# Kernel optimization log

Measured on AMD Instinct MI355X. Metric: run time of the kernel, lower is better.

Reference implementation:

```python
import jax, jax.numpy as jnp
import numpy as np

B, L, E = 2, 2048, 1024
H = 16
DH = E // H  # head dim for qk and v (dim_qk=dim_v=embed_dim)
HID = 4 * E  # fcn_dim_factor * dim_v
SCALE = DH ** 0.5


def setup_inputs() -> dict:
    key = jax.random.key(0)
    ks = jax.random.split(key, 12)
    s = lambda fan_in: 1.0 / np.sqrt(fan_in)
    return {
        "x": jax.random.uniform(ks[0], (B, L), jnp.float32),
        "z": jax.random.normal(ks[1], (B, L, E), jnp.float32),
        "Wq": jax.random.normal(ks[2], (E, E), jnp.float32) * s(E),
        "bq": jnp.zeros((E,), jnp.float32),
        "Wk": jax.random.normal(ks[3], (E, E), jnp.float32) * s(E),
        "bk": jnp.zeros((E,), jnp.float32),
        "Wv": jax.random.normal(ks[4], (E, E), jnp.float32) * s(E),
        "bv": jnp.zeros((E,), jnp.float32),
        "W1": jax.random.normal(ks[5], (E, HID), jnp.float32) * s(E),
        "b1": jnp.zeros((HID,), jnp.float32),
        "W2": jax.random.normal(ks[6], (HID, 1), jnp.float32) * s(HID),
        "b2": jnp.zeros((1,), jnp.float32),
    }


def reference(x, z, Wq, bq, Wk, bk, Wv, bv, W1, b1, W2, b2):
    # Projections -> (B, H, L, DH)
    def heads(t):
        return t.reshape(B, L, H, DH).transpose(0, 2, 1, 3)

    Q = heads(z @ Wq + bq)
    K = heads(z @ Wk + bk)
    V = heads(z @ Wv + bv)

    # Scores (B, H, L, L)
    S = jnp.einsum("bhid,bhjd->bhij", Q, K) / SCALE

    # Weighted softmax along query axis (dim=-2), weighted by population x
    w = x[:, None, :, None]  # (B, 1, L, 1), broadcasts over queries i
    m = jnp.max(S, axis=-2, keepdims=True)
    e = w * jnp.exp(S - m)
    A = e / jnp.sum(e, axis=-2, keepdims=True)

    # V scaled by population weight, then AV
    V_scaled = w * V
    O = jnp.einsum("bhij,bhjd->bhid", A, V_scaled)  # (B, H, L, DH)
    O = O.transpose(0, 2, 1, 3).reshape(B, L, H * DH)

    # FFN: Linear -> GELU (exact) -> Linear(->1) -> squeeze
    y = jax.nn.gelu(O @ W1 + b1, approximate=False)
    y = (y @ W2 + b2).squeeze(-1)  # (B, L)
    return y
```

## Files before the change

kernel.cpp:

```cpp
#include <hip/hip_runtime.h>
#include <hip/hip_bf16.h>
#include <math.h>

#define B_    2
#define L_    2048
#define E_    1024
#define H_    16
#define DH_   64
#define HID_  4096
#define NROW_ (B_*L_)
#define BH_   (B_*H_)

#define QSCL  0.18033688011112042f

typedef __attribute__((ext_vector_type(8)))  short    short8v;
typedef _Float16 half8v __attribute__((ext_vector_type(8)));
typedef __attribute__((ext_vector_type(16))) float    f32x16;

#define MFMA32(A, Bv, C) __builtin_amdgcn_mfma_f32_32x32x16_bf16((A), (Bv), (C), 0, 0, 0)
#define MFMAH(A, Bv, C)  __builtin_amdgcn_mfma_f32_32x32x16_f16((A), (Bv), (C), 0, 0, 0)

#define WAITV(N) asm volatile("s_waitcnt vmcnt(" #N ")" ::: "memory")
#define SBAR()   __builtin_amdgcn_s_barrier()

__device__ __forceinline__ unsigned short f2bf(float f) {
    union { float f; unsigned u; } v; v.f = f;
    return (unsigned short)((v.u + 0x8000u) >> 16);
}
__device__ __forceinline__ unsigned pack2_bf16(float lo, float hi) {
    union { float f; unsigned u; } a, b; a.f = lo; b.f = hi;
    return __builtin_amdgcn_perm(b.u + 0x8000u, a.u + 0x8000u, 0x07060302u);
}
__device__ __forceinline__ float bf2f(unsigned short u) {
    union { unsigned u; float f; } v; v.u = ((unsigned)u) << 16;
    return v.f;
}

__device__ __forceinline__ void gl_lds16(const void* g, void* l) {
    __builtin_amdgcn_global_load_lds(
        (const __attribute__((address_space(1))) unsigned int*)g,
        (__attribute__((address_space(3))) unsigned int*)l, 16, 0, 0);
}

__device__ __forceinline__ float erf_fast(float v) {
    float a = fabsf(v);
    float t = __builtin_amdgcn_rcpf(1.0f + 0.3275911f * a);
    float p = t * (0.254829592f + t * (-0.284496736f + t * (1.421413741f +
              t * (-1.453152027f + t * 1.061405429f))));
    float r = 1.0f - p * __expf(-a * a);
    return copysignf(r, v);
}

__global__ __launch_bounds__(256) void zh_prep(
    const float* __restrict__ z, _Float16* __restrict__ zh)
{
    const size_t i = ((size_t)blockIdx.x * 256 + threadIdx.x) * 8;
    float4 a = *(const float4*)&z[i];
    float4 b = *(const float4*)&z[i + 4];
    union { _Float16 h[8]; half8v v; } o;
    o.h[0] = (_Float16)a.x; o.h[1] = (_Float16)a.y;
    o.h[2] = (_Float16)a.z; o.h[3] = (_Float16)a.w;
    o.h[4] = (_Float16)b.x; o.h[5] = (_Float16)b.y;
    o.h[6] = (_Float16)b.z; o.h[7] = (_Float16)b.w;
    *(half8v*)&zh[i] = o.v;
}

__global__ __launch_bounds__(256) void wprep3(
    const float* __restrict__ Wq, const float* __restrict__ Wk,
    const float* __restrict__ Wv,
    _Float16* __restrict__ Tq, _Float16* __restrict__ Tk,
    _Float16* __restrict__ Tv)
{
    const float* src = (blockIdx.z == 0) ? Wq : (blockIdx.z == 1) ? Wk : Wv;
    _Float16*    dst = (blockIdx.z == 0) ? Tq : (blockIdx.z == 1) ? Tk : Tv;
    __shared__ float tile[64][65];
    const int t  = threadIdx.x;
    const int r0 = blockIdx.y * 64, c0 = blockIdx.x * 64;
    #pragma unroll
    for (int u = 0; u < 4; ++u) {
        int f = t + 256 * u, row = f >> 4, c4 = (f & 15) << 2;
        *(float4*)&tile[row][c4] = *(const float4*)&src[(size_t)(r0 + row) * E_ + c0 + c4];
    }
    __syncthreads();
    #pragma unroll
    for (int u = 0; u < 4; ++u) {
        int f = t + 256 * u, c = f >> 4, r4 = (f & 15) << 2;
        union { _Float16 h[4]; uint2 u2; } pk;
        pk.h[0] = (_Float16)tile[r4 + 0][c];
        pk.h[1] = (_Float16)tile[r4 + 1][c];
        pk.h[2] = (_Float16)tile[r4 + 2][c];
        pk.h[3] = (_Float16)tile[r4 + 3][c];
        *(uint2*)&dst[(size_t)(c0 + c) * E_ + r0 + r4] = pk.u2;
    }
}

__global__ __launch_bounds__(256) void w1prep(
    const float* __restrict__ W1, _Float16* __restrict__ W1t)
{
    __shared__ float tile[64][65];
    const int t  = threadIdx.x;
    const int r0 = blockIdx.y * 64, c0 = blockIdx.x * 64;
    #pragma unroll
    for (int u = 0; u < 4; ++u) {
        int f = t + 256 * u, row = f >> 4, c4 = (f & 15) << 2;
        *(float4*)&tile[row][c4] = *(const float4*)&W1[(size_t)(r0 + row) * HID_ + c0 + c4];
    }
    __syncthreads();
    #pragma unroll
    for (int u = 0; u < 4; ++u) {
        int f = t + 256 * u, c = f >> 4, r4 = (f & 15) << 2;
        union { _Float16 h[4]; uint2 u2; } pk;
        pk.h[0] = (_Float16)tile[r4 + 0][c];
        pk.h[1] = (_Float16)tile[r4 + 1][c];
        pk.h[2] = (_Float16)tile[r4 + 2][c];
        pk.h[3] = (_Float16)tile[r4 + 3][c];
        *(uint2*)&W1t[(size_t)(c0 + c) * E_ + r0 + r4] = pk.u2;
    }
}

__global__ __launch_bounds__(256) void qkv_mfma(
    const _Float16* __restrict__ zh,
    const _Float16* __restrict__ Tall,
    const float* __restrict__ bq, const float* __restrict__ bk,
    const float* __restrict__ bv,
    unsigned short* __restrict__ outQKV)
{
    const int which = blockIdx.y >> 3;
    const float* bias = (which == 0) ? bq : (which == 1) ? bk : bv;
    const float  osc  = (which == 0) ? QSCL : 1.0f;
    unsigned short* out = outQKV + (size_t)which * ((size_t)BH_ * L_ * DH_);

    __shared__ _Float16 Ah[2][128 * 64];
    __shared__ _Float16 Bs[2][128 * 64];

    const int t    = threadIdx.x;
    const int lane = t & 63;
    const int w    = t >> 6;
    const int l31  = lane & 31;
    const int hq   = lane >> 5;
    const int wm   = w >> 1, wn = w & 1;
    const int m0   = blockIdx.x * 128;
    const int n0   = blockIdx.y * 128;

    const int srow0 = (lane >> 3);
    const int ssl   = lane & 7;

    f32x16 acc[2][2] = {};

#define QKV_STAGE(bb, kc)                                                          \
    {                                                                              \
        _Pragma("unroll")                                                          \
        for (int u = 0; u < 4; ++u) {                                              \
            int ch  = w * 4 + u;                                                   \
            int row = ch * 8 + srow0;                                              \
            gl_lds16(&zh[(size_t)(m0 + row) * E_ + (kc) * 64 + ((ssl ^ (row & 7)) << 3)], \
                     &Ah[bb][ch * 512]);                                           \
            gl_lds16(&Tall[(size_t)(n0 + row) * E_ + (kc) * 64 + ((ssl ^ (row & 7)) << 3)], \
                     &Bs[bb][ch * 512]);                                           \
        }                                                                          \
    }

    QKV_STAGE(0, 0);
    QKV_STAGE(1, 1);
    __syncthreads();
    int cur = 0;

    for (int kc = 0; kc < 16; ++kc) {
        if (kc < 15) WAITV(8); else WAITV(0);
        SBAR();
        __builtin_amdgcn_s_setprio(1);
        #pragma unroll
        for (int ks = 0; ks < 4; ++ks) {
            half8v fb[2];
            #pragma unroll
            for (int nb = 0; nb < 2; ++nb) {
                int br = wn * 64 + nb * 32 + l31;
                fb[nb] = *(const half8v*)&Bs[cur][br * 64 + (((ks * 2 + hq) ^ (br & 7)) << 3)];
            }
            #pragma unroll
            for (int mb = 0; mb < 2; ++mb) {
                int ar = wm * 64 + mb * 32 + l31;
                half8v fa = *(const half8v*)&Ah[cur][ar * 64 + (((ks * 2 + hq) ^ (ar & 7)) << 3)];
                acc[mb][0] = MFMAH(fa, fb[0], acc[mb][0]);
                acc[mb][1] = MFMAH(fa, fb[1], acc[mb][1]);
            }
        }
        __builtin_amdgcn_s_setprio(0);
        SBAR();
        if (kc + 2 < 16) QKV_STAGE(cur, kc + 2);
        cur ^= 1;
    }

    #pragma unroll
    for (int nb = 0; nb < 2; ++nb) {
        int n  = n0 + wn * 64 + nb * 32 + l31;
        int nn = n & 1023;
        int h  = nn >> 6, dh = nn & 63;
        float bb = bias[nn];
        #pragma unroll
        for (int mb = 0; mb < 2; ++mb) {
            #pragma unroll
            for (int r = 0; r < 16; ++r) {
                int m  = m0 + wm * 64 + mb * 32 + (r & 3) + 8 * (r >> 2) + 4 * hq;
                int b  = m >> 11, i = m & (L_ - 1);
                out[((size_t)(b * H_ + h) * L_ + i) * DH_ + dh] = f2bf((acc[mb][nb][r] + bb) * osc);
            }
        }
    }
#undef QKV_STAGE
}

__global__ __launch_bounds__(256) void col_stats_mfma(
    const unsigned short* __restrict__ Qb, const unsigned short* __restrict__ Kb,
    const float* __restrict__ x, float* __restrict__ Do)
{
    __shared__ unsigned short Qlds[2][128 * 64];
    __shared__ float xlds[L_];

    const int t    = threadIdx.x;
    const int lane = t & 63;
    const int wv   = t >> 6;
    const int l31  = lane & 31;
    const int hq   = lane >> 5;
    const int bh   = blockIdx.y;
    const int b    = bh >> 4;
    const int j0   = blockIdx.x * 256 + wv * 64;

    const int srow0 = (lane >> 3);
    const int ssl   = lane & 7;

    #pragma unroll
    for (int u = 0; u < 2; ++u) {
        int f = t + 256 * u;
        *(float4*)&xlds[f * 4] = *(const float4*)&x[(size_t)b * L_ + f * 4];
    }

    short8v kf[2][4];
    #pragma unroll
    for (int s = 0; s < 2; ++s) {
        const unsigned short* kp = Kb + ((size_t)bh * L_ + j0 + s * 32 + l31) * DH_ + hq * 8;
        #pragma unroll
        for (int c = 0; c < 4; ++c) kf[s][c] = *(const short8v*)(kp + c * 16);
    }

    float d0[16], d1[16];
    #pragma unroll
    for (int r = 0; r < 16; ++r) { d0[r] = 0.f; d1[r] = 0.f; }

#define CS_STAGE(bb, ich)                                                           \
    {                                                                               \
        _Pragma("unroll")                                                           \
        for (int u = 0; u < 4; ++u) {                                               \
            int ch  = wv * 4 + u;                                                   \
            int row = ch * 8 + srow0;                                               \
            gl_lds16(&Qb[((size_t)bh * L_ + (ich) * 128 + row) * DH_ + ((ssl ^ (row & 7)) << 3)], \
                     &Qlds[bb][ch * 512]);                                          \
        }                                                                           \
    }

    CS_STAGE(0, 0);
    CS_STAGE(1, 1);
    __syncthreads();
    int cur = 0;

    const int NT = L_ / 128;
    for (int ich = 0; ich < NT; ++ich) {
        if (ich < NT - 1) WAITV(4); else WAITV(0);
        SBAR();
        #pragma unroll
        for (int cc = 0; cc < 4; ++cc) {
            f32x16 a0 = {}, a1 = {};
            __builtin_amdgcn_s_setprio(1);
            #pragma unroll
            for (int c = 0; c < 4; ++c) {
                int qr = cc * 32 + l31;
                short8v qv = *(const short8v*)&Qlds[cur][qr * 64 + (((c * 2 + hq) ^ (qr & 7)) << 3)];
                a0 = MFMA32(kf[0][c], qv, a0);
                a1 = MFMA32(kf[1][c], qv, a1);
            }
            __builtin_amdgcn_s_setprio(0);
            float xi = xlds[ich * 128 + cc * 32 + l31];
            #pragma unroll
            for (int r = 0; r < 16; ++r) {
                d0[r] += xi * __builtin_amdgcn_exp2f(a0[r]);
                d1[r] += xi * __builtin_amdgcn_exp2f(a1[r]);
            }
        }
        SBAR();
        if (ich + 2 < NT) CS_STAGE(cur, ich + 2);
        cur ^= 1;
    }

    #pragma unroll
    for (int r = 0; r < 16; ++r) {
        #pragma unroll
        for (int off = 16; off > 0; off >>= 1) {
            d0[r] += __shfl_xor(d0[r], off);
            d1[r] += __shfl_xor(d1[r], off);
        }
    }
    if (l31 == 0) {
        #pragma unroll
        for (int r = 0; r < 16; ++r) {
            int jr = 4 * hq + (r & 3) + 8 * (r >> 2);
            Do[(size_t)bh * L_ + j0 + jr]      = d0[r];
            Do[(size_t)bh * L_ + j0 + 32 + jr] = d1[r];
        }
    }
#undef CS_STAGE
}

__global__ __launch_bounds__(256) void vt_prep(
    const unsigned short* __restrict__ Vb, const float* __restrict__ x,
    const float* __restrict__ Do, unsigned short* __restrict__ Vt)
{
    const int bh = blockIdx.y;
    const int b  = bh >> 4;
    const int j  = blockIdx.x * 256 + threadIdx.x;
    const float s = x[(size_t)b * L_ + j] / Do[(size_t)bh * L_ + j];
    const unsigned short* vp = Vb + ((size_t)bh * L_ + j) * DH_;
    #pragma unroll
    for (int c = 0; c < 16; ++c) {
        ushort4 v = *(const ushort4*)&vp[c * 4];
        Vt[((size_t)bh * DH_ + c * 4 + 0) * L_ + j] = f2bf(bf2f(v.x) * s);
        Vt[((size_t)bh * DH_ + c * 4 + 1) * L_ + j] = f2bf(bf2f(v.y) * s);
        Vt[((size_t)bh * DH_ + c * 4 + 2) * L_ + j] = f2bf(bf2f(v.z) * s);
        Vt[((size_t)bh * DH_ + c * 4 + 3) * L_ + j] = f2bf(bf2f(v.w) * s);
    }
}

__global__ __launch_bounds__(512) void attn_out_mfma(
    const unsigned short* __restrict__ Qb, const unsigned short* __restrict__ Kb,
    const unsigned short* __restrict__ Vt, const float* __restrict__ x,
    _Float16* __restrict__ Of)
{
    __shared__ unsigned short Klds[2][2][64 * 64];
    __shared__ unsigned short Vlds[2][2][64 * 64];
    __shared__ float comb[4][64 * 67];

    const int t    = threadIdx.x;
    const int lane = t & 63;
    const int wv   = t >> 6;
    const int iwv  = wv & 3;
    const int jh   = wv >> 2;
    const int l31  = lane & 31;
    const int hq   = lane >> 5;
    const int bh   = blockIdx.y;
    const int b    = bh >> 4, hh = bh & 15;
    const int iw   = blockIdx.x * 256 + iwv * 64;

    const int srow0 = (lane >> 3);
    const int ssl   = lane & 7;

    short8v qf[2][4];
    #pragma unroll
    for (int ig = 0; ig < 2; ++ig) {
        const unsigned short* qp = Qb + ((size_t)bh * L_ + iw + ig * 32 + l31) * DH_ + hq * 8;
        #pragma unroll
        for (int c = 0; c < 4; ++c) qf[ig][c] = *(const short8v*)(qp + c * 16);
    }

    f32x16 accO[2][2] = {};

#define AO_STAGE(bb, jt)                                                            \
    {                                                                               \
        _Pragma("unroll")                                                           \
        for (int u = 0; u < 2; ++u) {                                               \
            int ch  = iwv * 2 + u;                                                  \
            int row = ch * 8 + srow0;                                               \
            gl_lds16(&Kb[((size_t)bh * L_ + (jt) * 64 + row) * DH_ + ((ssl ^ (row & 7)) << 3)], \
                     &Klds[jh][bb][ch * 512]);                                      \
            gl_lds16(&Vt[((size_t)bh * DH_ + row) * L_ + (jt) * 64 + ((ssl ^ (row & 7)) << 3)], \
                     &Vlds[jh][bb][ch * 512]);                                      \
        }                                                                           \
    }

    AO_STAGE(0, jh * 16 + 0);
    AO_STAGE(1, jh * 16 + 1);
    __syncthreads();
    int cur = 0;

    for (int ltj = 0; ltj < 16; ++ltj) {
        if (ltj < 15) WAITV(4); else WAITV(0);
        SBAR();

        uint4 pa[2][4];
        #pragma unroll
        for (int js = 0; js < 2; ++js) {
            f32x16 as0 = {}, as1 = {};
            __builtin_amdgcn_s_setprio(1);
            #pragma unroll
            for (int c = 0; c < 4; ++c) {
                int krow = js * 32 + l31;
                short8v kfr = *(const short8v*)&Klds[jh][cur][krow * 64 + (((c * 2 + hq) ^ (krow & 7)) << 3)];
                as0 = MFMA32(kfr, qf[0][c], as0);
                as1 = MFMA32(kfr, qf[1][c], as1);
            }
            __builtin_amdgcn_s_setprio(0);
            #pragma unroll
            for (int ig = 0; ig < 2; ++ig) {
                const f32x16& as = (ig == 0) ? as0 : as1;
                float p[16];
                #pragma unroll
                for (int r = 0; r < 16; ++r) p[r] = __builtin_amdgcn_exp2f(as[r]);

                unsigned P0 = pack2_bf16(p[0], p[1]);
                unsigned P1 = pack2_bf16(p[2], p[3]);
                unsigned Q0 = pack2_bf16(p[4], p[5]);
                unsigned Q1 = pack2_bf16(p[6], p[7]);
                asm("v_permlane32_swap_b32 %0, %1" : "+v"(P0), "+v"(Q0));
                asm("v_permlane32_swap_b32 %0, %1" : "+v"(P1), "+v"(Q1));
                pa[ig][js * 2 + 0] = make_uint4(P0, P1, Q0, Q1);

                unsigned R0 = pack2_bf16(p[8],  p[9]);
                unsigned R1 = pack2_bf16(p[10], p[11]);
                unsigned S0 = pack2_bf16(p[12], p[13]);
                unsigned S1 = pack2_bf16(p[14], p[15]);
                asm("v_permlane32_swap_b32 %0, %1" : "+v"(R0), "+v"(S0));
                asm("v_permlane32_swap_b32 %0, %1" : "+v"(R1), "+v"(S1));
                pa[ig][js * 2 + 1] = make_uint4(R0, R1, S0, S1);
            }
        }

        __builtin_amdgcn_s_setprio(1);
        #pragma unroll
        for (int c = 0; c < 4; ++c) {
            union { uint4 u; short8v s; } pa0, pa1;
            pa0.u = pa[0][c]; pa1.u = pa[1][c];
            int r0 = l31, r1 = 32 + l31;
            short8v vf0 = *(const short8v*)&Vlds[jh][cur][r0 * 64 + (((c * 2 + hq) ^ (r0 & 7)) << 3)];
            short8v vf1 = *(const short8v*)&Vlds[jh][cur][r1 * 64 + (((c * 2 + hq) ^ (r1 & 7)) << 3)];
            accO[0][0] = MFMA32(pa0.s, vf0, accO[0][0]);
            accO[0][1] = MFMA32(pa0.s, vf1, accO[0][1]);
            accO[1][0] = MFMA32(pa1.s, vf0, accO[1][0]);
            accO[1][1] = MFMA32(pa1.s, vf1, accO[1][1]);
        }
        __builtin_amdgcn_s_setprio(0);
        SBAR();
        if (ltj + 2 < 16) AO_STAGE(cur, jh * 16 + ltj + 2);
        cur ^= 1;
    }

    if (jh == 1) {
        float* cb = &comb[iwv][lane * 67];
        #pragma unroll
        for (int g = 0; g < 2; ++g)
            #pragma unroll
            for (int h = 0; h < 2; ++h)
                #pragma unroll
                for (int r = 0; r < 16; ++r)
                    cb[(g * 2 + h) * 16 + r] = accO[g][h][r];
    }
    __syncthreads();
    if (jh == 0) {
        const float* cb = &comb[iwv][lane * 67];
        #pragma unroll
        for (int g = 0; g < 2; ++g)
            #pragma unroll
            for (int h = 0; h < 2; ++h)
                #pragma unroll
                for (int r = 0; r < 16; ++r)
                    accO[g][h][r] += cb[(g * 2 + h) * 16 + r];

        #pragma unroll
        for (int ig = 0; ig < 2; ++ig) {
            #pragma unroll
            for (int q = 0; q < 4; ++q) {
                float4 xq = *(const float4*)&x[(size_t)b * L_ + iw + ig * 32 + 4 * hq + 8 * q];
                const float xs[4] = { xq.x, xq.y, xq.z, xq.w };
                #pragma unroll
                for (int k = 0; k < 4; ++k) {
                    int r    = q * 4 + k;
                    int irow = iw + ig * 32 + 4 * hq + 8 * q + k;
                    size_t base = ((size_t)b * L_ + irow) * E_ + hh * DH_;
                    Of[base + l31]      = (_Float16)(accO[ig][0][r] * xs[k]);
                    Of[base + 32 + l31] = (_Float16)(accO[ig][1][r] * xs[k]);
                }
            }
        }
    }
#undef AO_STAGE
}

__global__ __launch_bounds__(256) void y_init(float* __restrict__ y, const float* __restrict__ b2)
{
    y[blockIdx.x * 256 + threadIdx.x] = b2[0];
}

__global__ __launch_bounds__(256) void mlp_mfma(
    const _Float16* __restrict__ Of, const _Float16* __restrict__ W1t,
    const float* __restrict__ b1, const float* __restrict__ W2,
    float* __restrict__ y)
{
    __shared__ _Float16 Oh[2][128 * 64];
    __shared__ _Float16 Wh[2][128 * 64];

    const int t    = threadIdx.x;
    const int lane = t & 63;
    const int w    = t >> 6;
    const int l31  = lane & 31;
    const int hq   = lane >> 5;
    const int wm   = w >> 1, wn = w & 1;
    const int m0   = blockIdx.x * 128;
    const int n0   = blockIdx.y * 128;

    const int srow0 = (lane >> 3);
    const int ssl   = lane & 7;

    f32x16 acc[2][2] = {};

#define MLP_STAGE(bb, kc)                                                          \
    {                                                                              \
        _Pragma("unroll")                                                          \
        for (int u = 0; u < 4; ++u) {                                              \
            int ch  = w * 4 + u;                                                   \
            int row = ch * 8 + srow0;                                              \
            gl_lds16(&Of[(size_t)(m0 + row) * E_ + (kc) * 64 + ((ssl ^ (row & 7)) << 3)], \
                     &Oh[bb][ch * 512]);                                           \
            gl_lds16(&W1t[(size_t)(n0 + row) * E_ + (kc) * 64 + ((ssl ^ (row & 7)) << 3)], \
                     &Wh[bb][ch * 512]);                                           \
        }                                                                          \
    }

    MLP_STAGE(0, 0);
    MLP_STAGE(1, 1);
    __syncthreads();
    int cur = 0;

    for (int kc = 0; kc < 16; ++kc) {
        if (kc < 15) WAITV(8); else WAITV(0);
        SBAR();
        __builtin_amdgcn_s_setprio(1);
        #pragma unroll
        for (int ks = 0; ks < 4; ++ks) {
            half8v fb[2];
            #pragma unroll
            for (int nb = 0; nb < 2; ++nb) {
                int br = wn * 64 + nb * 32 + l31;
                fb[nb] = *(const half8v*)&Wh[cur][br * 64 + (((ks * 2 + hq) ^ (br & 7)) << 3)];
            }
            #pragma unroll
            for (int mb = 0; mb < 2; ++mb) {
                int ar = wm * 64 + mb * 32 + l31;
                half8v fa = *(const half8v*)&Oh[cur][ar * 64 + (((ks * 2 + hq) ^ (ar & 7)) << 3)];
                acc[mb][0] = MFMAH(fa, fb[0], acc[mb][0]);
                acc[mb][1] = MFMAH(fa, fb[1], acc[mb][1]);
            }
        }
        __builtin_amdgcn_s_setprio(0);
        SBAR();
        if (kc + 2 < 16) MLP_STAGE(cur, kc + 2);
        cur ^= 1;
    }

    const int hid0 = n0 + wn * 64 + l31;
    const float bb0 = b1[hid0],      w20 = W2[hid0];
    const float bb1 = b1[hid0 + 32], w21 = W2[hid0 + 32];
    #pragma unroll
    for (int mb = 0; mb < 2; ++mb) {
        #pragma unroll
        for (int r = 0; r < 16; ++r) {
            float h0 = acc[mb][0][r] + bb0;
            float h1 = acc[mb][1][r] + bb1;
            float s  = 0.5f * h0 * (1.0f + erf_fast(h0 * 0.70710678f)) * w20
                     + 0.5f * h1 * (1.0f + erf_fast(h1 * 0.70710678f)) * w21;
            #pragma unroll
            for (int off = 16; off > 0; off >>= 1) s += __shfl_xor(s, off);
            if (l31 == 0) {
                int m = m0 + wm * 64 + mb * 32 + (r & 3) + 8 * (r >> 2) + 4 * hq;
                atomicAdd(&y[m], s);
            }
        }
    }
#undef MLP_STAGE
}

extern "C" void kernel_launch(void* const* d_in, const int* in_sizes, int n_in,
                              void* d_out, int out_size, void* d_ws, size_t ws_size,
                              hipStream_t stream)
{
    const float* x  = (const float*)d_in[0];
    const float* z  = (const float*)d_in[1];
    const float* Wq = (const float*)d_in[2];
    const float* bq = (const float*)d_in[3];
    const float* Wk = (const float*)d_in[4];
    const float* bk = (const float*)d_in[5];
    const float* Wv = (const float*)d_in[6];
    const float* bv = (const float*)d_in[7];
    const float* W1 = (const float*)d_in[8];
    const float* b1 = (const float*)d_in[9];
    const float* W2 = (const float*)d_in[10];
    const float* b2 = (const float*)d_in[11];
    float* y = (float*)d_out;

    const size_t NQ = (size_t)BH_ * L_ * DH_;
    unsigned short* p = (unsigned short*)d_ws;
    unsigned short* Qb  = p;  p += NQ;
    unsigned short* Kb  = p;  p += NQ;
    unsigned short* Vb  = p;  p += NQ;
    unsigned short* Vt  = p;  p += NQ;
    _Float16* zh  = (_Float16*)p;  p += (size_t)NROW_ * E_;
    _Float16* Tq  = (_Float16*)p;  p += (size_t)E_ * E_;
    _Float16* Tk  = (_Float16*)p;  p += (size_t)E_ * E_;
    _Float16* Tv  = (_Float16*)p;  p += (size_t)E_ * E_;
    _Float16* W1t = (_Float16*)p;  p += (size_t)HID_ * E_;
    _Float16* Ofp = (_Float16*)p;  p += (size_t)NROW_ * E_;
    float* Dw = (float*)p;

    zh_prep<<<dim3((NROW_ * E_) / (256 * 8)), 256, 0, stream>>>(z, zh);
    wprep3 <<<dim3(E_ / 64, E_ / 64, 3), 256, 0, stream>>>(Wq, Wk, Wv, Tq, Tk, Tv);
    w1prep <<<dim3(HID_ / 64, E_ / 64), 256, 0, stream>>>(W1, W1t);

    qkv_mfma<<<dim3(NROW_ / 128, 3 * E_ / 128), 256, 0, stream>>>(
        zh, Tq, bq, bk, bv, Qb);

    col_stats_mfma<<<dim3(L_ / 256, BH_), 256, 0, stream>>>(Qb, Kb, x, Dw);

    vt_prep<<<dim3(L_ / 256, BH_), 256, 0, stream>>>(Vb, x, Dw, Vt);

    attn_out_mfma<<<dim3(L_ / 256, BH_), 512, 0, stream>>>(Qb, Kb, Vt, x, Ofp);

    y_init<<<dim3(NROW_ / 256), 256, 0, stream>>>(y, b2);

    mlp_mfma<<<dim3(NROW_ / 128, HID_ / 128), 256, 0, stream>>>(
        Ofp, W1t, b1, W2, y);
}
```

Baseline: 207.1 us.

## Split col_stats query range across two wave groups, tile vt_prep transpose, fold y init

col_stats_mfma now runs 512 threads per block, and the query axis is split into two halves handled by separate wave groups. The partial column sums are combined through shared memory, which doubles the waves per block to hide exp and MFMA latency. vt_prep becomes an LDS-tiled transpose with 16-byte vectorized loads and stores, replacing scattered 2-byte strided writes. The y_init kernel is dropped: y is zeroed with a memset and b2 is added by the first column block of mlp_mfma.

```diff
diff --git a/kernel.cpp b/kernel.cpp
--- a/kernel.cpp
+++ b/kernel.cpp
@@ -210,29 +210,30 @@
 #undef QKV_STAGE
 }
 
-__global__ __launch_bounds__(256) void col_stats_mfma(
+__global__ __launch_bounds__(512) void col_stats_mfma(
     const unsigned short* __restrict__ Qb, const unsigned short* __restrict__ Kb,
     const float* __restrict__ x, float* __restrict__ Do)
 {
-    __shared__ unsigned short Qlds[2][128 * 64];
+    __shared__ unsigned short Qlds[2][2][128 * 64];
     __shared__ float xlds[L_];
+    __shared__ float cD[4][64];
 
     const int t    = threadIdx.x;
     const int lane = t & 63;
     const int wv   = t >> 6;
+    const int jwv  = wv & 3;
+    const int ih   = wv >> 2;
     const int l31  = lane & 31;
     const int hq   = lane >> 5;
     const int bh   = blockIdx.y;
     const int b    = bh >> 4;
-    const int j0   = blockIdx.x * 256 + wv * 64;
+    const int j0   = blockIdx.x * 256 + jwv * 64;
 
     const int srow0 = (lane >> 3);
     const int ssl   = lane & 7;
 
-    #pragma unroll
-    for (int u = 0; u < 2; ++u) {
-        int f = t + 256 * u;
-        *(float4*)&xlds[f * 4] = *(const float4*)&x[(size_t)b * L_ + f * 4];
+    {
+        *(float4*)&xlds[t * 4] = *(const float4*)&x[(size_t)b * L_ + t * 4];
     }
 
     short8v kf[2][4];
@@ -247,14 +248,14 @@
     #pragma unroll
     for (int r = 0; r < 16; ++r) { d0[r] = 0.f; d1[r] = 0.f; }
 
-#define CS_STAGE(bb, ich)                                                           \
+#define CS_STAGE(bb, lt)                                                            \
     {                                                                               \
         _Pragma("unroll")                                                           \
         for (int u = 0; u < 4; ++u) {                                               \
-            int ch  = wv * 4 + u;                                                   \
+            int ch  = jwv * 4 + u;                                                  \
             int row = ch * 8 + srow0;                                               \
-            gl_lds16(&Qb[((size_t)bh * L_ + (ich) * 128 + row) * DH_ + ((ssl ^ (row & 7)) << 3)], \
-                     &Qlds[bb][ch * 512]);                                          \
+            gl_lds16(&Qb[((size_t)bh * L_ + (size_t)(ih * 8 + (lt)) * 128 + row) * DH_ + ((ssl ^ (row & 7)) << 3)], \
+                     &Qlds[ih][bb][ch * 512]);                                      \
         }                                                                           \
     }
 
@@ -263,9 +264,8 @@
     __syncthreads();
     int cur = 0;
 
-    const int NT = L_ / 128;
-    for (int ich = 0; ich < NT; ++ich) {
-        if (ich < NT - 1) WAITV(4); else WAITV(0);
+    for (int lt = 0; lt < 8; ++lt) {
+        if (lt < 7) WAITV(4); else WAITV(0);
         SBAR();
         #pragma unroll
         for (int cc = 0; cc < 4; ++cc) {
@@ -274,12 +274,12 @@
             #pragma unroll
             for (int c = 0; c < 4; ++c) {
                 int qr = cc * 32 + l31;
-                short8v qv = *(const short8v*)&Qlds[cur][qr * 64 + (((c * 2 + hq) ^ (qr & 7)) << 3)];
+                short8v qv = *(const short8v*)&Qlds[ih][cur][qr * 64 + (((c * 2 + hq) ^ (qr & 7)) << 3)];
                 a0 = MFMA32(kf[0][c], qv, a0);
                 a1 = MFMA32(kf[1][c], qv, a1);
             }
             __builtin_amdgcn_s_setprio(0);
-            float xi = xlds[ich * 128 + cc * 32 + l31];
+            float xi = xlds[(ih * 8 + lt) * 128 + cc * 32 + l31];
             #pragma unroll
             for (int r = 0; r < 16; ++r) {
                 d0[r] += xi * __builtin_amdgcn_exp2f(a0[r]);
@@ -287,7 +287,7 @@
             }
         }
         SBAR();
-        if (ich + 2 < NT) CS_STAGE(cur, ich + 2);
+        if (lt + 2 < 8) CS_STAGE(cur, lt + 2);
         cur ^= 1;
     }
 
@@ -299,12 +299,21 @@
             d1[r] += __shfl_xor(d1[r], off);
         }
     }
-    if (l31 == 0) {
+    if (ih == 1 && l31 == 0) {
         #pragma unroll
         for (int r = 0; r < 16; ++r) {
             int jr = 4 * hq + (r & 3) + 8 * (r >> 2);
-            Do[(size_t)bh * L_ + j0 + jr]      = d0[r];
-            Do[(size_t)bh * L_ + j0 + 32 + jr] = d1[r];
+            cD[jwv][jr]      = d0[r];
+            cD[jwv][32 + jr] = d1[r];
+        }
+    }
+    __syncthreads();
+    if (ih == 0 && l31 == 0) {
+        #pragma unroll
+        for (int r = 0; r < 16; ++r) {
+            int jr = 4 * hq + (r & 3) + 8 * (r >> 2);
+            Do[(size_t)bh * L_ + j0 + jr]      = d0[r] + cD[jwv][jr];
+            Do[(size_t)bh * L_ + j0 + 32 + jr] = d1[r] + cD[jwv][32 + jr];
         }
     }
 #undef CS_STAGE
@@ -314,18 +323,41 @@
     const unsigned short* __restrict__ Vb, const float* __restrict__ x,
     const float* __restrict__ Do, unsigned short* __restrict__ Vt)
 {
+    __shared__ float sc[64];
+    __shared__ unsigned short vt[64][66];
+
+    const int t  = threadIdx.x;
     const int bh = blockIdx.y;
     const int b  = bh >> 4;
-    const int j  = blockIdx.x * 256 + threadIdx.x;
-    const float s = x[(size_t)b * L_ + j] / Do[(size_t)bh * L_ + j];
-    const unsigned short* vp = Vb + ((size_t)bh * L_ + j) * DH_;
-    #pragma unroll
-    for (int c = 0; c < 16; ++c) {
-        ushort4 v = *(const ushort4*)&vp[c * 4];
-        Vt[((size_t)bh * DH_ + c * 4 + 0) * L_ + j] = f2bf(bf2f(v.x) * s);
-        Vt[((size_t)bh * DH_ + c * 4 + 1) * L_ + j] = f2bf(bf2f(v.y) * s);
-        Vt[((size_t)bh * DH_ + c * 4 + 2) * L_ + j] = f2bf(bf2f(v.z) * s);
-        Vt[((size_t)bh * DH_ + c * 4 + 3) * L_ + j] = f2bf(bf2f(v.w) * s);
+    const int j0 = blockIdx.x * 64;
+
+    if (t < 64) {
+        int j = j0 + t;
+        sc[t] = x[(size_t)b * L_ + j] / Do[(size_t)bh * L_ + j];
+    }
+    __syncthreads();
+
+    #pragma unroll
+    for (int u = 0; u < 2; ++u) {
+        int idx = t + 256 * u;
+        int row = idx >> 3, off = (idx & 7) * 8;
+        short8v v = *(const short8v*)&Vb[((size_t)bh * L_ + j0 + row) * DH_ + off];
+        float s = sc[row];
+        const unsigned short* vs = (const unsigned short*)&v;
+        #pragma unroll
+        for (int k = 0; k < 8; ++k)
+            vt[row][off + k] = f2bf(bf2f(vs[k]) * s);
+    }
+    __syncthreads();
+
+    #pragma unroll
+    for (int u = 0; u < 2; ++u) {
+        int idx = t + 256 * u;
+        int dh = idx >> 3, js = (idx & 7) * 8;
+        unsigned short o[8];
+        #pragma unroll
+        for (int k = 0; k < 8; ++k) o[k] = vt[js + k][dh];
+        *(short8v*)&Vt[((size_t)bh * DH_ + dh) * L_ + j0 + js] = *(const short8v*)o;
     }
 }
 
@@ -482,15 +514,10 @@
 #undef AO_STAGE
 }
 
-__global__ __launch_bounds__(256) void y_init(float* __restrict__ y, const float* __restrict__ b2)
-{
-    y[blockIdx.x * 256 + threadIdx.x] = b2[0];
-}
-
 __global__ __launch_bounds__(256) void mlp_mfma(
     const _Float16* __restrict__ Of, const _Float16* __restrict__ W1t,
     const float* __restrict__ b1, const float* __restrict__ W2,
-    float* __restrict__ y)
+    const float* __restrict__ b2, float* __restrict__ y)
 {
     __shared__ _Float16 Oh[2][128 * 64];
     __shared__ _Float16 Wh[2][128 * 64];
@@ -556,6 +583,7 @@
     const int hid0 = n0 + wn * 64 + l31;
     const float bb0 = b1[hid0],      w20 = W2[hid0];
     const float bb1 = b1[hid0 + 32], w21 = W2[hid0 + 32];
+    const float b2v = (blockIdx.y == 0) ? b2[0] : 0.0f;
     #pragma unroll
     for (int mb = 0; mb < 2; ++mb) {
         #pragma unroll
@@ -568,7 +596,7 @@
             for (int off = 16; off > 0; off >>= 1) s += __shfl_xor(s, off);
             if (l31 == 0) {
                 int m = m0 + wm * 64 + mb * 32 + (r & 3) + 8 * (r >> 2) + 4 * hq;
-                atomicAdd(&y[m], s);
+                atomicAdd(&y[m], s + b2v);
             }
         }
     }
@@ -607,6 +635,8 @@
     _Float16* Ofp = (_Float16*)p;  p += (size_t)NROW_ * E_;
     float* Dw = (float*)p;
 
+    hipMemsetAsync(y, 0, (size_t)out_size * sizeof(float), stream);
+
     zh_prep<<<dim3((NROW_ * E_) / (256 * 8)), 256, 0, stream>>>(z, zh);
     wprep3 <<<dim3(E_ / 64, E_ / 64, 3), 256, 0, stream>>>(Wq, Wk, Wv, Tq, Tk, Tv);
     w1prep <<<dim3(HID_ / 64, E_ / 64), 256, 0, stream>>>(W1, W1t);
@@ -614,14 +644,12 @@
     qkv_mfma<<<dim3(NROW_ / 128, 3 * E_ / 128), 256, 0, stream>>>(
         zh, Tq, bq, bk, bv, Qb);
 
-    col_stats_mfma<<<dim3(L_ / 256, BH_), 256, 0, stream>>>(Qb, Kb, x, Dw);
-
-    vt_prep<<<dim3(L_ / 256, BH_), 256, 0, stream>>>(Vb, x, Dw, Vt);
+    col_stats_mfma<<<dim3(L_ / 256, BH_), 512, 0, stream>>>(Qb, Kb, x, Dw);
+
+    vt_prep<<<dim3(L_ / 64, BH_), 256, 0, stream>>>(Vb, x, Dw, Vt);
 
     attn_out_mfma<<<dim3(L_ / 256, BH_), 512, 0, stream>>>(Qb, Kb, Vt, x, Ofp);
 
-    y_init<<<dim3(NROW_ / 256), 256, 0, stream>>>(y, b2);
-
     mlp_mfma<<<dim3(NROW_ / 128, HID_ / 128), 256, 0, stream>>>(
-        Ofp, W1t, b1, W2, y);
-}
+        Ofp, W1t, b1, W2, b2, y);
+}
```

New measurement: 204.8 us. About the same (-1.1%).
